# Kernel tuning notes

Hardware: AMD Instinct MI355X
Metric: run time of the kernel (lower is better)

## Reference

```python
import jax, jax.numpy as jnp
import numpy as np
import math

B, T, C = 2, 2048, 2048
H, KV, HD = 16, 4, 128          # n_head, n_kv_head, head_dim
REP = H // KV
FFN = 5632                      # multiple_of-rounded 2/3 * 4 * n_embd
EPS = 1e-5


def setup_inputs() -> dict:
    key = jax.random.key(0)
    ks = jax.random.split(key, 10)
    s = 0.02
    x = jax.random.normal(ks[0], (B, T, C), dtype=jnp.float32)
    # RoPE table: (T, HD/2, 2) = (cos, sin)
    inv_freq = 1.0 / (10000.0 ** (np.arange(0, HD, 2, dtype=np.float32) / HD))
    ang = np.arange(T, dtype=np.float32)[:, None] * inv_freq[None, :]
    freqs_cis = jnp.asarray(np.stack([np.cos(ang), np.sin(ang)], axis=-1))
    wq = s * jax.random.normal(ks[1], (H * HD, C), dtype=jnp.float32)
    wk = s * jax.random.normal(ks[2], (KV * HD, C), dtype=jnp.float32)
    wv = s * jax.random.normal(ks[3], (KV * HD, C), dtype=jnp.float32)
    wo = s * jax.random.normal(ks[4], (C, H * HD), dtype=jnp.float32)
    w1 = s * jax.random.normal(ks[5], (FFN, C), dtype=jnp.float32)
    w2 = s * jax.random.normal(ks[6], (FFN, C), dtype=jnp.float32)
    c_proj = s * jax.random.normal(ks[7], (C, FFN), dtype=jnp.float32)
    g1 = jnp.ones((C,), dtype=jnp.float32)
    g2 = jnp.ones((C,), dtype=jnp.float32)
    return {"x": x, "freqs_cis": freqs_cis, "wq": wq, "wk": wk, "wv": wv,
            "wo": wo, "w1": w1, "w2": w2, "c_proj": c_proj, "g1": g1, "g2": g2}


def _rmsnorm(x, g, eps=EPS):
    return x * jax.lax.rsqrt(jnp.mean(x * x, axis=-1, keepdims=True) + eps) * g


def _rope(t, freqs_cis):
    # t: (B, T, nH, HD); freqs_cis: (T, HD/2, 2)
    tr = t.reshape(*t.shape[:-1], HD // 2, 2)
    cos = freqs_cis[None, :, None, :, 0]
    sin = freqs_cis[None, :, None, :, 1]
    out = jnp.stack([tr[..., 0] * cos - tr[..., 1] * sin,
                     tr[..., 0] * sin + tr[..., 1] * cos], axis=-1)
    return out.reshape(t.shape)


def reference(x, freqs_cis, wq, wk, wv, wo, w1, w2, c_proj, g1, g2):
    h = _rmsnorm(x, g1)
    q = (h @ wq.T).reshape(B, T, H, HD)
    k = (h @ wk.T).reshape(B, T, KV, HD)
    v = (h @ wv.T).reshape(B, T, KV, HD)
    q = _rope(q, freqs_cis)
    k = _rope(k, freqs_cis)
    # GQA: group query heads by kv head; never materialize expanded K/V
    q = q.transpose(0, 2, 1, 3).reshape(B, KV, REP, T, HD)  # b g r q d
    k = k.transpose(0, 2, 1, 3)                              # b g k d
    v = v.transpose(0, 2, 1, 3)                              # b g k d
    scale = 1.0 / math.sqrt(HD)
    scores = jnp.einsum('bgrqd,bgkd->bgrqk', q, k) * scale
    causal = jnp.tril(jnp.ones((T, T), dtype=bool))
    scores = jnp.where(causal, scores, jnp.float32(-1e30))
    attn = jax.nn.softmax(scores, axis=-1)
    y = jnp.einsum('bgrqk,bgkd->bgrqd', attn, v)
    y = y.reshape(B, H, T, HD).transpose(0, 2, 1, 3).reshape(B, T, C)
    x = x + y @ wo.T
    h2 = _rmsnorm(x, g2)
    mlp = (jax.nn.silu(h2 @ w1.T) * (h2 @ w2.T)) @ c_proj.T
    return x + mlp
```

## Files before the change

kernel.cpp:

```cpp
#include <hip/hip_runtime.h>
#include <hip/hip_bf16.h>
#include <math.h>

#define TT   2048
#define CC   2048
#define NB   2
#define NH   16
#define NKV  4
#define HDIM 128
#define NFFN 5632

typedef __attribute__((ext_vector_type(8))) short     bf8;
typedef __attribute__((ext_vector_type(4))) float     f32x4;
typedef __attribute__((ext_vector_type(8))) unsigned short u16x8;
typedef __attribute__((ext_vector_type(4))) unsigned short u16x4;

__device__ __forceinline__ float b2f(unsigned short u) {
    union { unsigned u; float f; } v; v.u = ((unsigned)u) << 16; return v.f;
}
__device__ __forceinline__ unsigned short f2bf(float f) {
    union { float f; unsigned u; } v; v.f = f;
    unsigned r = (v.u + 0x7fffu + ((v.u >> 16) & 1u)) >> 16;
    return (unsigned short)r;
}
__device__ __forceinline__ void gll16(const void* g, void* l) {
    __builtin_amdgcn_global_load_lds((const __attribute__((address_space(1))) void*)g,
                                     (__attribute__((address_space(3))) void*)l, 16, 0, 0);
}

__global__ __launch_bounds__(256) void cvt_k(const float* __restrict__ in,
        __hip_bfloat16* __restrict__ out)
{
    const size_t i = ((size_t)blockIdx.x * 256 + threadIdx.x) * 8;
    float4 a = *(const float4*)(in + i);
    float4 b = *(const float4*)(in + i + 4);
    u16x8 v;
    v[0] = f2bf(a.x); v[1] = f2bf(a.y); v[2] = f2bf(a.z); v[3] = f2bf(a.w);
    v[4] = f2bf(b.x); v[5] = f2bf(b.y); v[6] = f2bf(b.z); v[7] = f2bf(b.w);
    *(u16x8*)((unsigned short*)out + i) = v;
}

__global__ __launch_bounds__(256) void cvt3_k(const float* __restrict__ wq,
        const float* __restrict__ wk, const float* __restrict__ wv,
        __hip_bfloat16* __restrict__ out)
{
    const int row = blockIdx.x;
    const float* src = (row < 2048) ? (wq + (size_t)row * CC)
                     : (row < 2560) ? (wk + (size_t)(row - 2048) * CC)
                                    : (wv + (size_t)(row - 2560) * CC);
    const int e0 = threadIdx.x * 8;
    float4 a = *(const float4*)(src + e0);
    float4 b = *(const float4*)(src + e0 + 4);
    u16x8 v;
    v[0] = f2bf(a.x); v[1] = f2bf(a.y); v[2] = f2bf(a.z); v[3] = f2bf(a.w);
    v[4] = f2bf(b.x); v[5] = f2bf(b.y); v[6] = f2bf(b.z); v[7] = f2bf(b.w);
    *(u16x8*)((unsigned short*)out + (size_t)row * CC + e0) = v;
}

__global__ __launch_bounds__(256) void cvt2_k(const float* __restrict__ w1,
        const float* __restrict__ w2,
        __hip_bfloat16* __restrict__ o1, __hip_bfloat16* __restrict__ o2)
{
    const int row = blockIdx.x;
    const float* src;
    unsigned short* dst;
    if (row < NFFN) { src = w1 + (size_t)row * CC; dst = (unsigned short*)o1 + (size_t)row * CC; }
    else            { src = w2 + (size_t)(row - NFFN) * CC; dst = (unsigned short*)o2 + (size_t)(row - NFFN) * CC; }
    const int e0 = threadIdx.x * 8;
    float4 a = *(const float4*)(src + e0);
    float4 b = *(const float4*)(src + e0 + 4);
    u16x8 v;
    v[0] = f2bf(a.x); v[1] = f2bf(a.y); v[2] = f2bf(a.z); v[3] = f2bf(a.w);
    v[4] = f2bf(b.x); v[5] = f2bf(b.y); v[6] = f2bf(b.z); v[7] = f2bf(b.w);
    *(u16x8*)(dst + e0) = v;
}

__global__ __launch_bounds__(256) void rms_f32_k(const float* __restrict__ x,
        const float* __restrict__ g, __hip_bfloat16* __restrict__ o)
{
    const size_t row = blockIdx.x;
    const int e0 = threadIdx.x * 8;
    float4 a = *(const float4*)(x + row * CC + e0);
    float4 b = *(const float4*)(x + row * CC + e0 + 4);
    float vals[8] = {a.x, a.y, a.z, a.w, b.x, b.y, b.z, b.w};
    float s = 0.f;
    #pragma unroll
    for (int e = 0; e < 8; ++e) s += vals[e] * vals[e];
    #pragma unroll
    for (int off = 32; off; off >>= 1) s += __shfl_xor(s, off);
    __shared__ float wsum[4];
    if ((threadIdx.x & 63) == 0) wsum[threadIdx.x >> 6] = s;
    __syncthreads();
    float scale = rsqrtf((wsum[0] + wsum[1] + wsum[2] + wsum[3]) * (1.0f / CC) + 1e-5f);
    float4 g0 = *(const float4*)(g + e0);
    float4 g1 = *(const float4*)(g + e0 + 4);
    float gs[8] = {g0.x, g0.y, g0.z, g0.w, g1.x, g1.y, g1.z, g1.w};
    u16x8 ov;
    #pragma unroll
    for (int e = 0; e < 8; ++e) ov[e] = f2bf(vals[e] * scale * gs[e]);
    *(u16x8*)((unsigned short*)o + row * CC + e0) = ov;
}

__global__ __launch_bounds__(256) void rms_bf16_k(const __hip_bfloat16* __restrict__ x,
        const float* __restrict__ g, __hip_bfloat16* __restrict__ o)
{
    const size_t row = blockIdx.x;
    const int e0 = threadIdx.x * 8;
    u16x8 xv = *(const u16x8*)((const unsigned short*)x + row * CC + e0);
    float vals[8];
    #pragma unroll
    for (int e = 0; e < 8; ++e) vals[e] = b2f(xv[e]);
    float s = 0.f;
    #pragma unroll
    for (int e = 0; e < 8; ++e) s += vals[e] * vals[e];
    #pragma unroll
    for (int off = 32; off; off >>= 1) s += __shfl_xor(s, off);
    __shared__ float wsum[4];
    if ((threadIdx.x & 63) == 0) wsum[threadIdx.x >> 6] = s;
    __syncthreads();
    float scale = rsqrtf((wsum[0] + wsum[1] + wsum[2] + wsum[3]) * (1.0f / CC) + 1e-5f);
    float4 g0 = *(const float4*)(g + e0);
    float4 g1 = *(const float4*)(g + e0 + 4);
    float gs[8] = {g0.x, g0.y, g0.z, g0.w, g1.x, g1.y, g1.z, g1.w};
    u16x8 ov;
    #pragma unroll
    for (int e = 0; e < 8; ++e) ov[e] = f2bf(vals[e] * scale * gs[e]);
    *(u16x8*)((unsigned short*)o + row * CC + e0) = ov;
}

#define GBM 128
#define GBN 128
#define GBK 32

template<int EPI, int OUTB>
__global__ __launch_bounds__(256) void gemm_db(
        const __hip_bfloat16* __restrict__ A,
        const __hip_bfloat16* __restrict__ W,
        const void* __restrict__ Rp,
        void* __restrict__ Cp,
        int M, int N, int K)
{
    __shared__ alignas(16) __hip_bfloat16 As[2][GBM][GBK];
    __shared__ alignas(16) __hip_bfloat16 Ws[2][GBN][GBK];
    const int tid  = threadIdx.x;
    const int lane = tid & 63;
    const int wid  = tid >> 6;
    const int wr = wid >> 1, wc = wid & 1;
    const int nwg = gridDim.x * gridDim.y;
    const int lin = blockIdx.y * gridDim.x + blockIdx.x;
    const int nlin = (lin & 7) * (nwg >> 3) + (lin >> 3);
    const int bxs = nlin % gridDim.x, bys = nlin / gridDim.x;
    const int bm = bys * GBM, bn = bxs * GBN;
    const int l4  = lane >> 2;
    const int lk8 = (lane & 3) * 8;
    const int fr  = lane & 15;
    const int fk  = (lane >> 4) * 8;

    f32x4 acc[4][4];
    #pragma unroll
    for (int m = 0; m < 4; ++m)
        #pragma unroll
        for (int n = 0; n < 4; ++n) acc[m][n] = (f32x4){0.f, 0.f, 0.f, 0.f};

    const __hip_bfloat16* ga0 = A + (size_t)(bm + wid * 32 + l4) * K + lk8;
    const __hip_bfloat16* ga1 = A + (size_t)(bm + wid * 32 + 16 + l4) * K + lk8;
    const __hip_bfloat16* gw0 = W + (size_t)(bn + wid * 32 + l4) * K + lk8;
    const __hip_bfloat16* gw1 = W + (size_t)(bn + wid * 32 + 16 + l4) * K + lk8;

    const int nt = K >> 5;
    gll16(ga0, &As[0][wid * 32][0]);
    gll16(ga1, &As[0][wid * 32 + 16][0]);
    gll16(gw0, &Ws[0][wid * 32][0]);
    gll16(gw1, &Ws[0][wid * 32 + 16][0]);

    #pragma unroll 2
    for (int t = 0; t < nt; ++t) {
        const int cur = t & 1;
        __syncthreads();
        if (t + 1 < nt) {
            const int k1 = (t + 1) << 5;
            const int nx = cur ^ 1;
            gll16(ga0 + k1, &As[nx][wid * 32][0]);
            gll16(ga1 + k1, &As[nx][wid * 32 + 16][0]);
            gll16(gw0 + k1, &Ws[nx][wid * 32][0]);
            gll16(gw1 + k1, &Ws[nx][wid * 32 + 16][0]);
        }
        bf8 af[4];
        #pragma unroll
        for (int m = 0; m < 4; ++m)
            af[m] = *(const bf8*)&As[cur][wr * 64 + m * 16 + fr][fk];
        #pragma unroll
        for (int n = 0; n < 4; ++n) {
            bf8 wf = *(const bf8*)&Ws[cur][wc * 64 + n * 16 + fr][fk];
            #pragma unroll
            for (int m = 0; m < 4; ++m)
                acc[m][n] = __builtin_amdgcn_mfma_f32_16x16x32_bf16(af[m], wf, acc[m][n], 0, 0, 0);
        }
    }

    const int rj = (lane >> 4) * 4;
    #pragma unroll
    for (int m = 0; m < 4; ++m) {
        #pragma unroll
        for (int j = 0; j < 4; ++j) {
            const size_t row = (size_t)(bm + wr * 64 + m * 16 + rj + j);
            #pragma unroll
            for (int n = 0; n < 4; ++n) {
                const size_t col = (size_t)(bn + wc * 64 + n * 16 + fr);
                float v = acc[m][n][j];
                if (EPI == 1) v += ((const float*)Rp)[row * N + col];
                if (EPI == 2) v += b2f(((const unsigned short*)Rp)[row * N + col]);
                if (EPI == 3) {
                    float gv = b2f(((const unsigned short*)Rp)[row * N + col]);
                    v = (gv / (1.0f + __expf(-gv))) * v;
                }
                if (OUTB) ((unsigned short*)Cp)[row * N + col] = f2bf(v);
                else      ((float*)Cp)[row * N + col] = v;
            }
        }
    }
}

__global__ __launch_bounds__(256) void gemm_qkv_db(
        const __hip_bfloat16* __restrict__ A,
        const __hip_bfloat16* __restrict__ W,
        const float* __restrict__ fc,
        __hip_bfloat16* __restrict__ qo,
        __hip_bfloat16* __restrict__ ko,
        __hip_bfloat16* __restrict__ vto,
        int M, int K)
{
    __shared__ alignas(16) __hip_bfloat16 As[2][GBM][GBK];
    __shared__ alignas(16) __hip_bfloat16 Ws[2][GBN][GBK];
    const int tid  = threadIdx.x;
    const int lane = tid & 63;
    const int wid  = tid >> 6;
    const int wr = wid >> 1, wc = wid & 1;
    const int nwg = gridDim.x * gridDim.y;
    const int lin = blockIdx.y * gridDim.x + blockIdx.x;
    const int nlin = (lin & 7) * (nwg >> 3) + (lin >> 3);
    const int bxs = nlin % gridDim.x, bys = nlin / gridDim.x;
    const int bm = bys * GBM, bn = bxs * GBN;
    const int l4  = lane >> 2;
    const int lk8 = (lane & 3) * 8;
    const int fr  = lane & 15;
    const int fk  = (lane >> 4) * 8;

    f32x4 acc[4][4];
    #pragma unroll
    for (int m = 0; m < 4; ++m)
        #pragma unroll
        for (int n = 0; n < 4; ++n) acc[m][n] = (f32x4){0.f, 0.f, 0.f, 0.f};

    const __hip_bfloat16* ga0 = A + (size_t)(bm + wid * 32 + l4) * K + lk8;
    const __hip_bfloat16* ga1 = A + (size_t)(bm + wid * 32 + 16 + l4) * K + lk8;
    const __hip_bfloat16* gw0 = W + (size_t)(bn + wid * 32 + l4) * K + lk8;
    const __hip_bfloat16* gw1 = W + (size_t)(bn + wid * 32 + 16 + l4) * K + lk8;

    const int nt = K >> 5;
    gll16(ga0, &As[0][wid * 32][0]);
    gll16(ga1, &As[0][wid * 32 + 16][0]);
    gll16(gw0, &Ws[0][wid * 32][0]);
    gll16(gw1, &Ws[0][wid * 32 + 16][0]);

    #pragma unroll 2
    for (int t = 0; t < nt; ++t) {
        const int cur = t & 1;
        __syncthreads();
        if (t + 1 < nt) {
            const int k1 = (t + 1) << 5;
            const int nx = cur ^ 1;
            gll16(ga0 + k1, &As[nx][wid * 32][0]);
            gll16(ga1 + k1, &As[nx][wid * 32 + 16][0]);
            gll16(gw0 + k1, &Ws[nx][wid * 32][0]);
            gll16(gw1 + k1, &Ws[nx][wid * 32 + 16][0]);
        }
        bf8 af[4];
        #pragma unroll
        for (int m = 0; m < 4; ++m)
            af[m] = *(const bf8*)&As[cur][wr * 64 + m * 16 + fr][fk];
        #pragma unroll
        for (int n = 0; n < 4; ++n) {
            bf8 wf = *(const bf8*)&Ws[cur][wc * 64 + n * 16 + fr][fk];
            #pragma unroll
            for (int m = 0; m < 4; ++m)
                acc[m][n] = __builtin_amdgcn_mfma_f32_16x16x32_bf16(af[m], wf, acc[m][n], 0, 0, 0);
        }
    }

    const int rj = (lane >> 4) * 4;
    #pragma unroll
    for (int m = 0; m < 4; ++m) {
        #pragma unroll
        for (int n = 0; n < 4; ++n) {
            const int col = bn + wc * 64 + n * 16 + fr;
            const int row0 = bm + wr * 64 + m * 16 + rj;
            if (col < 2560) {
                const int i2 = ((col & 127) >> 1) * 2;
                const int role = col & 1;
                #pragma unroll
                for (int j = 0; j < 4; ++j) {
                    const int t0 = (row0 + j) & (TT - 1);
                    const float cv = fc[t0 * HDIM + i2];
                    const float sv = fc[t0 * HDIM + i2 + 1];
                    const float v = acc[m][n][j];
                    const float partner = __shfl_xor(v, 1);
                    const float o = role ? (partner * sv + v * cv) : (v * cv - partner * sv);
                    if (col < 2048)
                        ((unsigned short*)qo)[(size_t)(row0 + j) * CC + col] = f2bf(o);
                    else
                        ((unsigned short*)ko)[(size_t)(row0 + j) * (NKV * HDIM) + (col - 2048)] = f2bf(o);
                }
            } else {
                const int vc = col - 2560;
                const int g = vc >> 7, d = vc & 127;
                const int b = row0 >> 11, t0 = row0 & (TT - 1);
                unsigned short* vp = (unsigned short*)vto +
                    ((size_t)(b * NKV + g) * HDIM + d) * TT + t0;
                u16x4 ov;
                #pragma unroll
                for (int j = 0; j < 4; ++j) ov[j] = f2bf(acc[m][n][j]);
                *(u16x4*)vp = ov;
            }
        }
    }
}

#define PBM 128
#define PBN 256
#define PBK 64

template<int EPI, int OUTB>
__global__ __launch_bounds__(512) void gemm_8p(
        const __hip_bfloat16* __restrict__ A,
        const __hip_bfloat16* __restrict__ W,
        const void* __restrict__ Rp,
        void* __restrict__ Cp,
        int M, int N, int K)
{
    __shared__ alignas(16) __hip_bfloat16 As[2][PBM][PBK];
    __shared__ alignas(16) __hip_bfloat16 Ws[2][PBN][PBK];
    const int tid  = threadIdx.x;
    const int lane = tid & 63;
    const int wid  = tid >> 6;
    const int wr = wid >> 2, wc = wid & 3;
    const int nwg = gridDim.x * gridDim.y;
    const int lin = blockIdx.y * gridDim.x + blockIdx.x;
    const int nlin = (lin & 7) * (nwg >> 3) + (lin >> 3);
    const int bxs = nlin % gridDim.x, bys = nlin / gridDim.x;
    const int bm = bys * PBM, bn = bxs * PBN;
    const int fr = lane & 15;
    const int hi = lane >> 4;

    f32x4 acc[4][4];
    #pragma unroll
    for (int m = 0; m < 4; ++m)
        #pragma unroll
        for (int n = 0; n < 4; ++n) acc[m][n] = (f32x4){0.f, 0.f, 0.f, 0.f};

    const unsigned short* Ag = (const unsigned short*)A;
    const unsigned short* Wg = (const unsigned short*)W;

    auto STAGE = [&](int buf, int k0) {
        #pragma unroll
        for (int l = 0; l < 2; ++l) {
            const int s = l * 512 + tid;
            const int row = s >> 3;
            const int srcb = ((s & 7) * 16) ^ ((row & 7) << 4);
            gll16(Ag + (size_t)(bm + row) * K + k0 + (srcb >> 1),
                  (unsigned short*)&As[buf][0][0] + (l * 512 + wid * 64) * 8);
        }
        #pragma unroll
        for (int l = 0; l < 4; ++l) {
            const int s = l * 512 + tid;
            const int row = s >> 3;
            const int srcb = ((s & 7) * 16) ^ ((row & 7) << 4);
            gll16(Wg + (size_t)(bn + row) * K + k0 + (srcb >> 1),
                  (unsigned short*)&Ws[buf][0][0] + (l * 512 + wid * 64) * 8);
        }
    };

    const int nt = K >> 6;
    STAGE(0, 0);
    __syncthreads();

    for (int t = 0; t < nt; ++t) {
        const int cur = t & 1;
        const char* Ab = (const char*)&As[cur][0][0];
        const char* Bb = (const char*)&Ws[cur][0][0];

        bf8 bF[4][2];
        #pragma unroll
        for (int n = 0; n < 4; ++n) {
            const int row = wc * 64 + n * 16 + fr;
            #pragma unroll
            for (int kk = 0; kk < 2; ++kk) {
                const int off = (kk * 64 + hi * 16) ^ ((row & 7) << 4);
                bF[n][kk] = *(const bf8*)(Bb + row * 128 + off);
            }
        }
        bf8 a0, a1;
        {
            const int row = wr * 64 + fr;
            a0 = *(const bf8*)(Ab + row * 128 + ((hi * 16)      ^ ((row & 7) << 4)));
            a1 = *(const bf8*)(Ab + row * 128 + ((64 + hi * 16) ^ ((row & 7) << 4)));
        }
        if (t + 1 < nt) STAGE(cur ^ 1, (t + 1) * PBK);
        __builtin_amdgcn_s_barrier();
        __builtin_amdgcn_s_setprio(1);
        #pragma unroll
        for (int n = 0; n < 4; ++n) {
            acc[0][n] = __builtin_amdgcn_mfma_f32_16x16x32_bf16(a0, bF[n][0], acc[0][n], 0, 0, 0);
            acc[0][n] = __builtin_amdgcn_mfma_f32_16x16x32_bf16(a1, bF[n][1], acc[0][n], 0, 0, 0);
        }
        __builtin_amdgcn_s_setprio(0);
        __builtin_amdgcn_s_barrier();

        #pragma unroll
        for (int m = 1; m < 4; ++m) {
            const int row = wr * 64 + m * 16 + fr;
            bf8 am0 = *(const bf8*)(Ab + row * 128 + ((hi * 16)      ^ ((row & 7) << 4)));
            bf8 am1 = *(const bf8*)(Ab + row * 128 + ((64 + hi * 16) ^ ((row & 7) << 4)));
            __builtin_amdgcn_s_barrier();
            __builtin_amdgcn_s_setprio(1);
            #pragma unroll
            for (int n = 0; n < 4; ++n) {
                acc[m][n] = __builtin_amdgcn_mfma_f32_16x16x32_bf16(am0, bF[n][0], acc[m][n], 0, 0, 0);
                acc[m][n] = __builtin_amdgcn_mfma_f32_16x16x32_bf16(am1, bF[n][1], acc[m][n], 0, 0, 0);
            }
            __builtin_amdgcn_s_setprio(0);
            if (m < 3) __builtin_amdgcn_s_barrier();
        }
        __syncthreads();
    }

    const int rj = hi * 4;
    #pragma unroll
    for (int m = 0; m < 4; ++m) {
        #pragma unroll
        for (int j = 0; j < 4; ++j) {
            const size_t row = (size_t)(bm + wr * 64 + m * 16 + rj + j);
            #pragma unroll
            for (int n = 0; n < 4; ++n) {
                const size_t col = (size_t)(bn + wc * 64 + n * 16 + fr);
                float v = acc[m][n][j];
                if (EPI == 1) v += ((const float*)Rp)[row * N + col];
                if (EPI == 2) v += b2f(((const unsigned short*)Rp)[row * N + col]);
                if (EPI == 3) {
                    float gv = b2f(((const unsigned short*)Rp)[row * N + col]);
                    v = (gv / (1.0f + __expf(-gv))) * v;
                }
                if (OUTB) ((unsigned short*)Cp)[row * N + col] = f2bf(v);
                else      ((float*)Cp)[row * N + col] = v;
            }
        }
    }
}

#define AQB 128
#define AKV 64

__global__ __launch_bounds__(512) void attn_mfma(const __hip_bfloat16* __restrict__ q,
        const __hip_bfloat16* __restrict__ k, const __hip_bfloat16* __restrict__ vt,
        __hip_bfloat16* __restrict__ y)
{
    __shared__ alignas(16) unsigned short Ks[AKV * HDIM];
    __shared__ alignas(16) unsigned short Vs[HDIM * AKV];
    __shared__ alignas(16) unsigned short Ps[AQB * AKV];

    const int qt = (TT / AQB - 1) - blockIdx.x;
    const int h  = blockIdx.y;
    const int b  = blockIdx.z;
    const int g  = h >> 2;
    const int qbase = qt * AQB;

    const int tid  = threadIdx.x;
    const int lane = tid & 63;
    const int wid  = tid >> 6;
    const int fr   = lane & 15;
    const int fk8  = (lane >> 4) * 8;
    const int rj   = (lane >> 4) * 4;

    bf8 qf[4];
    {
        const unsigned short* qp = (const unsigned short*)q +
            (size_t)(b * TT + qbase + wid * 16 + fr) * CC + h * HDIM;
        #pragma unroll
        for (int c = 0; c < 4; ++c)
            qf[c] = *(const bf8*)(qp + c * 32 + fk8);
    }
    const unsigned short* vtb = (const unsigned short*)vt + (size_t)(b * NKV + g) * HDIM * TT;

    f32x4 oacc[8];
    float m_r = -1e30f, l_r = 0.f;
    #pragma unroll
    for (int n = 0; n < 8; ++n) oacc[n] = (f32x4){0.f, 0.f, 0.f, 0.f};

    const float scale = 0.08838834764831845f;
    const int ntiles = qbase / AKV + 2;
    const int kjr = tid >> 3;
    const int kkc = (tid & 7) * 16;
    const int vdr = tid >> 2;
    const int vjc = (tid & 3) * 16;
    const int qg = qbase + wid * 16 + fr;
    const int prow = wid * 16 + fr;

    u16x8 krg[2], vrg[2];
    auto LOADT = [&](int jb) {
        const unsigned short* kp = (const unsigned short*)k +
            ((size_t)(b * TT + jb + kjr) * (NKV * HDIM)) + g * HDIM + kkc;
        const unsigned short* vp = vtb + (size_t)vdr * TT + jb + vjc;
        #pragma unroll
        for (int c = 0; c < 2; ++c) {
            krg[c] = *(const u16x8*)(kp + c * 8);
            vrg[c] = *(const u16x8*)(vp + c * 8);
        }
    };
    auto WRITET = [&]() {
        #pragma unroll
        for (int c = 0; c < 2; ++c) {
            const int byteK = (kjr * 256 + (kkc + c * 8) * 2) ^ ((kjr & 7) << 4);
            *(u16x8*)((char*)Ks + byteK) = krg[c];
            const int byteV = (vdr * 128 + (vjc + c * 8) * 2) ^ ((vdr & 7) << 4);
            *(u16x8*)((char*)Vs + byteV) = vrg[c];
        }
    };

    LOADT(0);

    for (int tile = 0; tile < ntiles; ++tile) {
        __syncthreads();
        WRITET();
        if (tile + 1 < ntiles) LOADT((tile + 1) * AKV);
        __syncthreads();

        f32x4 s[4];
        #pragma unroll
        for (int n = 0; n < 4; ++n) s[n] = (f32x4){0.f, 0.f, 0.f, 0.f};
        __builtin_amdgcn_s_setprio(1);
        #pragma unroll
        for (int c = 0; c < 4; ++c) {
            #pragma unroll
            for (int n = 0; n < 4; ++n) {
                const int j = n * 16 + fr;
                const int byteB = (j * 256 + (c * 32 + fk8) * 2) ^ ((j & 7) << 4);
                bf8 kf = *(const bf8*)((char*)Ks + byteB);
                s[n] = __builtin_amdgcn_mfma_f32_16x16x32_bf16(kf, qf[c], s[n], 0, 0, 0);
            }
        }
        __builtin_amdgcn_s_setprio(0);

        const int jbase = tile * AKV;
        float sv[4][4];
        float tmax = -1e30f;
        #pragma unroll
        for (int n = 0; n < 4; ++n)
            #pragma unroll
            for (int j = 0; j < 4; ++j) {
                const int jg = jbase + n * 16 + rj + j;
                sv[n][j] = (jg <= qg) ? s[n][j] * scale : -1e30f;
                tmax = fmaxf(tmax, sv[n][j]);
            }
        tmax = fmaxf(tmax, __shfl_xor(tmax, 16));
        tmax = fmaxf(tmax, __shfl_xor(tmax, 32));
        const bool trig = tmax > m_r + 8.0f;
        if (__any(trig)) {
            const float alpha = trig ? __expf(m_r - tmax) : 1.0f;
            if (trig) m_r = tmax;
            l_r *= alpha;
            float aj[4];
            #pragma unroll
            for (int j = 0; j < 4; ++j) aj[j] = __shfl(alpha, rj + j);
            #pragma unroll
            for (int n = 0; n < 8; ++n)
                #pragma unroll
                for (int j = 0; j < 4; ++j) oacc[n][j] *= aj[j];
        }
        float tsum = 0.f;
        #pragma unroll
        for (int n = 0; n < 4; ++n)
            #pragma unroll
            for (int j = 0; j < 4; ++j) {
                const float p = __expf(sv[n][j] - m_r);
                tsum += p;
                const int byteP = (prow * 128 + (n * 16 + rj + j) * 2) ^ ((prow & 7) << 4);
                *(unsigned short*)((char*)Ps + byteP) = f2bf(p);
            }
        tsum += __shfl_xor(tsum, 16);
        tsum += __shfl_xor(tsum, 32);
        l_r += tsum;

        __builtin_amdgcn_s_setprio(1);
        #pragma unroll
        for (int c2 = 0; c2 < 2; ++c2) {
            const int byteA = (prow * 128 + (c2 * 32 + fk8) * 2) ^ ((prow & 7) << 4);
            bf8 pf = *(const bf8*)((char*)Ps + byteA);
            #pragma unroll
            for (int n = 0; n < 8; ++n) {
                const int d = n * 16 + fr;
                const int byteB = (d * 128 + (c2 * 32 + fk8) * 2) ^ ((d & 7) << 4);
                bf8 vf = *(const bf8*)((char*)Vs + byteB);
                oacc[n] = __builtin_amdgcn_mfma_f32_16x16x32_bf16(pf, vf, oacc[n], 0, 0, 0);
            }
        }
        __builtin_amdgcn_s_setprio(0);
    }

    const float rl = 1.0f / l_r;
    #pragma unroll
    for (int jj = 0; jj < 4; ++jj) {
        const float inv = __shfl(rl, rj + jj);
        unsigned short* yrow = (unsigned short*)y +
            ((size_t)(b * TT + qbase + wid * 16 + rj + jj) * CC) + h * HDIM;
        #pragma unroll
        for (int n = 0; n < 8; ++n)
            yrow[n * 16 + fr] = f2bf(oacc[n][jj] * inv);
    }
}

extern "C" void kernel_launch(void* const* d_in, const int* in_sizes, int n_in,
                              void* d_out, int out_size, void* d_ws, size_t ws_size,
                              hipStream_t stream)
{
    (void)in_sizes; (void)n_in; (void)out_size; (void)ws_size;
    const float* x     = (const float*)d_in[0];
    const float* fc    = (const float*)d_in[1];
    const float* wq    = (const float*)d_in[2];
    const float* wk    = (const float*)d_in[3];
    const float* wv    = (const float*)d_in[4];
    const float* wo    = (const float*)d_in[5];
    const float* w1    = (const float*)d_in[6];
    const float* w2    = (const float*)d_in[7];
    const float* cproj = (const float*)d_in[8];
    const float* g1    = (const float*)d_in[9];
    const float* g2    = (const float*)d_in[10];
    float* out = (float*)d_out;

    const int ROWS = NB * TT;
    unsigned char* wsb = (unsigned char*)d_ws;
    __hip_bfloat16* x2b = (__hip_bfloat16*)(wsb);
    __hip_bfloat16* hb  = (__hip_bfloat16*)(wsb + 16777216u);
    __hip_bfloat16* w1b = (__hip_bfloat16*)(wsb + 33554432u);
    __hip_bfloat16* w2b = (__hip_bfloat16*)(wsb + 56623104u);
    __hip_bfloat16* G1  = (__hip_bfloat16*)(wsb + 79691776u);
    __hip_bfloat16* cpb = w1b;
    __hip_bfloat16* qb   = (__hip_bfloat16*)(wsb + 33554432u);
    __hip_bfloat16* kb   = (__hip_bfloat16*)(wsb + 50331648u);
    __hip_bfloat16* vtb  = (__hip_bfloat16*)(wsb + 54525952u);
    __hip_bfloat16* yb   = (__hip_bfloat16*)(wsb + 58720256u);
    __hip_bfloat16* wbuf = (__hip_bfloat16*)(wsb + 75497472u);

    rms_f32_k<<<ROWS, 256, 0, stream>>>(x, g1, hb);
    cvt3_k<<<3072, 256, 0, stream>>>(wq, wk, wv, wbuf);
    gemm_qkv_db<<<dim3(3072 / GBN, ROWS / GBM), 256, 0, stream>>>(hb, wbuf, fc, qb, kb, vtb, ROWS, CC);
    attn_mfma<<<dim3(TT / AQB, NH, NB), 512, 0, stream>>>(qb, kb, vtb, yb);
    cvt_k<<<(CC * CC) / 2048, 256, 0, stream>>>(wo, wbuf);
    gemm_8p<1, 1><<<dim3(CC / PBN, ROWS / PBM), 512, 0, stream>>>(yb, wbuf, x, x2b, ROWS, CC, CC);
    rms_bf16_k<<<ROWS, 256, 0, stream>>>(x2b, g2, hb);
    cvt2_k<<<2 * NFFN, 256, 0, stream>>>(w1, w2, w1b, w2b);
    gemm_8p<0, 1><<<dim3(NFFN / PBN, ROWS / PBM), 512, 0, stream>>>(hb, w1b, nullptr, G1, ROWS, NFFN, CC);
    gemm_8p<3, 1><<<dim3(NFFN / PBN, ROWS / PBM), 512, 0, stream>>>(hb, w2b, G1, G1, ROWS, NFFN, CC);
    cvt_k<<<(CC * NFFN) / 2048, 256, 0, stream>>>(cproj, cpb);
    gemm_8p<2, 0><<<dim3(CC / PBN, ROWS / PBM), 512, 0, stream>>>(G1, cpb, x2b, out, ROWS, CC, NFFN);
}
```

Before: 620.2 us.

## Port QKV GEMM to 8-wave pipelined kernel and double-buffer attention K/V tiles

The QKV projection GEMM moves from the 256-thread 128x128x32 double-buffered kernel to the 512-thread 128x256x64 design already used for the other GEMMs. That design uses swizzled LDS staging and interleaves barriers with MFMA groups. The old gemm_db is removed. The attention kernel now double-buffers its K/V shared-memory tiles and writes the next tile after the PV MFMAs, which drops one __syncthreads per tile and overlaps the LDS write with compute. In exchange, attention uses more LDS, and the QKV grid has fewer, larger blocks (12x32).

```diff
diff --git a/kernel.cpp b/kernel.cpp
--- a/kernel.cpp
+++ b/kernel.cpp
@@ -128,33 +128,31 @@
     *(u16x8*)((unsigned short*)o + row * CC + e0) = ov;
 }
 
-#define GBM 128
-#define GBN 128
-#define GBK 32
+#define PBM 128
+#define PBN 256
+#define PBK 64
 
 template<int EPI, int OUTB>
-__global__ __launch_bounds__(256) void gemm_db(
+__global__ __launch_bounds__(512) void gemm_8p(
         const __hip_bfloat16* __restrict__ A,
         const __hip_bfloat16* __restrict__ W,
         const void* __restrict__ Rp,
         void* __restrict__ Cp,
         int M, int N, int K)
 {
-    __shared__ alignas(16) __hip_bfloat16 As[2][GBM][GBK];
-    __shared__ alignas(16) __hip_bfloat16 Ws[2][GBN][GBK];
+    __shared__ alignas(16) __hip_bfloat16 As[2][PBM][PBK];
+    __shared__ alignas(16) __hip_bfloat16 Ws[2][PBN][PBK];
     const int tid  = threadIdx.x;
     const int lane = tid & 63;
     const int wid  = tid >> 6;
-    const int wr = wid >> 1, wc = wid & 1;
+    const int wr = wid >> 2, wc = wid & 3;
     const int nwg = gridDim.x * gridDim.y;
     const int lin = blockIdx.y * gridDim.x + blockIdx.x;
     const int nlin = (lin & 7) * (nwg >> 3) + (lin >> 3);
     const int bxs = nlin % gridDim.x, bys = nlin / gridDim.x;
-    const int bm = bys * GBM, bn = bxs * GBN;
-    const int l4  = lane >> 2;
-    const int lk8 = (lane & 3) * 8;
-    const int fr  = lane & 15;
-    const int fk  = (lane >> 4) * 8;
+    const int bm = bys * PBM, bn = bxs * PBN;
+    const int fr = lane & 15;
+    const int hi = lane >> 4;
 
     f32x4 acc[4][4];
     #pragma unroll
@@ -162,43 +160,83 @@
         #pragma unroll
         for (int n = 0; n < 4; ++n) acc[m][n] = (f32x4){0.f, 0.f, 0.f, 0.f};
 
-    const __hip_bfloat16* ga0 = A + (size_t)(bm + wid * 32 + l4) * K + lk8;
-    const __hip_bfloat16* ga1 = A + (size_t)(bm + wid * 32 + 16 + l4) * K + lk8;
-    const __hip_bfloat16* gw0 = W + (size_t)(bn + wid * 32 + l4) * K + lk8;
-    const __hip_bfloat16* gw1 = W + (size_t)(bn + wid * 32 + 16 + l4) * K + lk8;
-
-    const int nt = K >> 5;
-    gll16(ga0, &As[0][wid * 32][0]);
-    gll16(ga1, &As[0][wid * 32 + 16][0]);
-    gll16(gw0, &Ws[0][wid * 32][0]);
-    gll16(gw1, &Ws[0][wid * 32 + 16][0]);
-
-    #pragma unroll 2
+    const unsigned short* Ag = (const unsigned short*)A;
+    const unsigned short* Wg = (const unsigned short*)W;
+
+    auto STAGE = [&](int buf, int k0) {
+        #pragma unroll
+        for (int l = 0; l < 2; ++l) {
+            const int s = l * 512 + tid;
+            const int row = s >> 3;
+            const int srcb = ((s & 7) * 16) ^ ((row & 7) << 4);
+            gll16(Ag + (size_t)(bm + row) * K + k0 + (srcb >> 1),
+                  (unsigned short*)&As[buf][0][0] + (l * 512 + wid * 64) * 8);
+        }
+        #pragma unroll
+        for (int l = 0; l < 4; ++l) {
+            const int s = l * 512 + tid;
+            const int row = s >> 3;
+            const int srcb = ((s & 7) * 16) ^ ((row & 7) << 4);
+            gll16(Wg + (size_t)(bn + row) * K + k0 + (srcb >> 1),
+                  (unsigned short*)&Ws[buf][0][0] + (l * 512 + wid * 64) * 8);
+        }
+    };
+
+    const int nt = K >> 6;
+    STAGE(0, 0);
+    __syncthreads();
+
     for (int t = 0; t < nt; ++t) {
         const int cur = t & 1;
+        const char* Ab = (const char*)&As[cur][0][0];
+        const char* Bb = (const char*)&Ws[cur][0][0];
+
+        bf8 bF[4][2];
+        #pragma unroll
+        for (int n = 0; n < 4; ++n) {
+            const int row = wc * 64 + n * 16 + fr;
+            #pragma unroll
+            for (int kk = 0; kk < 2; ++kk) {
+                const int off = (kk * 64 + hi * 16) ^ ((row & 7) << 4);
+                bF[n][kk] = *(const bf8*)(Bb + row * 128 + off);
+            }
+        }
+        bf8 a0, a1;
+        {
+            const int row = wr * 64 + fr;
+            a0 = *(const bf8*)(Ab + row * 128 + ((hi * 16)      ^ ((row & 7) << 4)));
+            a1 = *(const bf8*)(Ab + row * 128 + ((64 + hi * 16) ^ ((row & 7) << 4)));
+        }
+        if (t + 1 < nt) STAGE(cur ^ 1, (t + 1) * PBK);
+        __builtin_amdgcn_s_barrier();
+        __builtin_amdgcn_s_setprio(1);
+        #pragma unroll
+        for (int n = 0; n < 4; ++n) {
+            acc[0][n] = __builtin_amdgcn_mfma_f32_16x16x32_bf16(a0, bF[n][0], acc[0][n], 0, 0, 0);
+            acc[0][n] = __builtin_amdgcn_mfma_f32_16x16x32_bf16(a1, bF[n][1], acc[0][n], 0, 0, 0);
+        }
+        __builtin_amdgcn_s_setprio(0);
+        __builtin_amdgcn_s_barrier();
+
+        #pragma unroll
+        for (int m = 1; m < 4; ++m) {
+            const int row = wr * 64 + m * 16 + fr;
+            bf8 am0 = *(const bf8*)(Ab + row * 128 + ((hi * 16)      ^ ((row & 7) << 4)));
+            bf8 am1 = *(const bf8*)(Ab + row * 128 + ((64 + hi * 16) ^ ((row & 7) << 4)));
+            __builtin_amdgcn_s_barrier();
+            __builtin_amdgcn_s_setprio(1);
+            #pragma unroll
+            for (int n = 0; n < 4; ++n) {
+                acc[m][n] = __builtin_amdgcn_mfma_f32_16x16x32_bf16(am0, bF[n][0], acc[m][n], 0, 0, 0);
+                acc[m][n] = __builtin_amdgcn_mfma_f32_16x16x32_bf16(am1, bF[n][1], acc[m][n], 0, 0, 0);
+            }
+            __builtin_amdgcn_s_setprio(0);
+            if (m < 3) __builtin_amdgcn_s_barrier();
+        }
         __syncthreads();
-        if (t + 1 < nt) {
-            const int k1 = (t + 1) << 5;
-            const int nx = cur ^ 1;
-            gll16(ga0 + k1, &As[nx][wid * 32][0]);
-            gll16(ga1 + k1, &As[nx][wid * 32 + 16][0]);
-            gll16(gw0 + k1, &Ws[nx][wid * 32][0]);
-            gll16(gw1 + k1, &Ws[nx][wid * 32 + 16][0]);
-        }
-        bf8 af[4];
-        #pragma unroll
-        for (int m = 0; m < 4; ++m)
-            af[m] = *(const bf8*)&As[cur][wr * 64 + m * 16 + fr][fk];
-        #pragma unroll
-        for (int n = 0; n < 4; ++n) {
-            bf8 wf = *(const bf8*)&Ws[cur][wc * 64 + n * 16 + fr][fk];
-            #pragma unroll
-            for (int m = 0; m < 4; ++m)
-                acc[m][n] = __builtin_amdgcn_mfma_f32_16x16x32_bf16(af[m], wf, acc[m][n], 0, 0, 0);
-        }
     }
 
-    const int rj = (lane >> 4) * 4;
+    const int rj = hi * 4;
     #pragma unroll
     for (int m = 0; m < 4; ++m) {
         #pragma unroll
@@ -221,7 +259,7 @@
     }
 }
 
-__global__ __launch_bounds__(256) void gemm_qkv_db(
+__global__ __launch_bounds__(512) void gemm_qkv_8p(
         const __hip_bfloat16* __restrict__ A,
         const __hip_bfloat16* __restrict__ W,
         const float* __restrict__ fc,
@@ -230,21 +268,19 @@
         __hip_bfloat16* __restrict__ vto,
         int M, int K)
 {
-    __shared__ alignas(16) __hip_bfloat16 As[2][GBM][GBK];
-    __shared__ alignas(16) __hip_bfloat16 Ws[2][GBN][GBK];
+    __shared__ alignas(16) __hip_bfloat16 As[2][PBM][PBK];
+    __shared__ alignas(16) __hip_bfloat16 Ws[2][PBN][PBK];
     const int tid  = threadIdx.x;
     const int lane = tid & 63;
     const int wid  = tid >> 6;
-    const int wr = wid >> 1, wc = wid & 1;
+    const int wr = wid >> 2, wc = wid & 3;
     const int nwg = gridDim.x * gridDim.y;
     const int lin = blockIdx.y * gridDim.x + blockIdx.x;
     const int nlin = (lin & 7) * (nwg >> 3) + (lin >> 3);
     const int bxs = nlin % gridDim.x, bys = nlin / gridDim.x;
-    const int bm = bys * GBM, bn = bxs * GBN;
-    const int l4  = lane >> 2;
-    const int lk8 = (lane & 3) * 8;
-    const int fr  = lane & 15;
-    const int fk  = (lane >> 4) * 8;
+    const int bm = bys * PBM, bn = bxs * PBN;
+    const int fr = lane & 15;
+    const int hi = lane >> 4;
 
     f32x4 acc[4][4];
     #pragma unroll
@@ -252,43 +288,83 @@
         #pragma unroll
         for (int n = 0; n < 4; ++n) acc[m][n] = (f32x4){0.f, 0.f, 0.f, 0.f};
 
-    const __hip_bfloat16* ga0 = A + (size_t)(bm + wid * 32 + l4) * K + lk8;
-    const __hip_bfloat16* ga1 = A + (size_t)(bm + wid * 32 + 16 + l4) * K + lk8;
-    const __hip_bfloat16* gw0 = W + (size_t)(bn + wid * 32 + l4) * K + lk8;
-    const __hip_bfloat16* gw1 = W + (size_t)(bn + wid * 32 + 16 + l4) * K + lk8;
-
-    const int nt = K >> 5;
-    gll16(ga0, &As[0][wid * 32][0]);
-    gll16(ga1, &As[0][wid * 32 + 16][0]);
-    gll16(gw0, &Ws[0][wid * 32][0]);
-    gll16(gw1, &Ws[0][wid * 32 + 16][0]);
-
-    #pragma unroll 2
+    const unsigned short* Ag = (const unsigned short*)A;
+    const unsigned short* Wg = (const unsigned short*)W;
+
+    auto STAGE = [&](int buf, int k0) {
+        #pragma unroll
+        for (int l = 0; l < 2; ++l) {
+            const int s = l * 512 + tid;
+            const int row = s >> 3;
+            const int srcb = ((s & 7) * 16) ^ ((row & 7) << 4);
+            gll16(Ag + (size_t)(bm + row) * K + k0 + (srcb >> 1),
+                  (unsigned short*)&As[buf][0][0] + (l * 512 + wid * 64) * 8);
+        }
+        #pragma unroll
+        for (int l = 0; l < 4; ++l) {
+            const int s = l * 512 + tid;
+            const int row = s >> 3;
+            const int srcb = ((s & 7) * 16) ^ ((row & 7) << 4);
+            gll16(Wg + (size_t)(bn + row) * K + k0 + (srcb >> 1),
+                  (unsigned short*)&Ws[buf][0][0] + (l * 512 + wid * 64) * 8);
+        }
+    };
+
+    const int nt = K >> 6;
+    STAGE(0, 0);
+    __syncthreads();
+
     for (int t = 0; t < nt; ++t) {
         const int cur = t & 1;
+        const char* Ab = (const char*)&As[cur][0][0];
+        const char* Bb = (const char*)&Ws[cur][0][0];
+
+        bf8 bF[4][2];
+        #pragma unroll
+        for (int n = 0; n < 4; ++n) {
+            const int row = wc * 64 + n * 16 + fr;
+            #pragma unroll
+            for (int kk = 0; kk < 2; ++kk) {
+                const int off = (kk * 64 + hi * 16) ^ ((row & 7) << 4);
+                bF[n][kk] = *(const bf8*)(Bb + row * 128 + off);
+            }
+        }
+        bf8 a0, a1;
+        {
+            const int row = wr * 64 + fr;
+            a0 = *(const bf8*)(Ab + row * 128 + ((hi * 16)      ^ ((row & 7) << 4)));
+            a1 = *(const bf8*)(Ab + row * 128 + ((64 + hi * 16) ^ ((row & 7) << 4)));
+        }
+        if (t + 1 < nt) STAGE(cur ^ 1, (t + 1) * PBK);
+        __builtin_amdgcn_s_barrier();
+        __builtin_amdgcn_s_setprio(1);
+        #pragma unroll
+        for (int n = 0; n < 4; ++n) {
+            acc[0][n] = __builtin_amdgcn_mfma_f32_16x16x32_bf16(a0, bF[n][0], acc[0][n], 0, 0, 0);
+            acc[0][n] = __builtin_amdgcn_mfma_f32_16x16x32_bf16(a1, bF[n][1], acc[0][n], 0, 0, 0);
+        }
+        __builtin_amdgcn_s_setprio(0);
+        __builtin_amdgcn_s_barrier();
+
+        #pragma unroll
+        for (int m = 1; m < 4; ++m) {
+            const int row = wr * 64 + m * 16 + fr;
+            bf8 am0 = *(const bf8*)(Ab + row * 128 + ((hi * 16)      ^ ((row & 7) << 4)));
+            bf8 am1 = *(const bf8*)(Ab + row * 128 + ((64 + hi * 16) ^ ((row & 7) << 4)));
+            __builtin_amdgcn_s_barrier();
+            __builtin_amdgcn_s_setprio(1);
+            #pragma unroll
+            for (int n = 0; n < 4; ++n) {
+                acc[m][n] = __builtin_amdgcn_mfma_f32_16x16x32_bf16(am0, bF[n][0], acc[m][n], 0, 0, 0);
+                acc[m][n] = __builtin_amdgcn_mfma_f32_16x16x32_bf16(am1, bF[n][1], acc[m][n], 0, 0, 0);
+            }
+            __builtin_amdgcn_s_setprio(0);
+            if (m < 3) __builtin_amdgcn_s_barrier();
+        }
         __syncthreads();
-        if (t + 1 < nt) {
-            const int k1 = (t + 1) << 5;
-            const int nx = cur ^ 1;
-            gll16(ga0 + k1, &As[nx][wid * 32][0]);
-            gll16(ga1 + k1, &As[nx][wid * 32 + 16][0]);
-            gll16(gw0 + k1, &Ws[nx][wid * 32][0]);
-            gll16(gw1 + k1, &Ws[nx][wid * 32 + 16][0]);
-        }
-        bf8 af[4];
-        #pragma unroll
-        for (int m = 0; m < 4; ++m)
-            af[m] = *(const bf8*)&As[cur][wr * 64 + m * 16 + fr][fk];
-        #pragma unroll
-        for (int n = 0; n < 4; ++n) {
-            bf8 wf = *(const bf8*)&Ws[cur][wc * 64 + n * 16 + fr][fk];
-            #pragma unroll
-            for (int m = 0; m < 4; ++m)
-                acc[m][n] = __builtin_amdgcn_mfma_f32_16x16x32_bf16(af[m], wf, acc[m][n], 0, 0, 0);
-        }
     }
 
-    const int rj = (lane >> 4) * 4;
+    const int rj = hi * 4;
     #pragma unroll
     for (int m = 0; m < 4; ++m) {
         #pragma unroll
@@ -326,137 +402,6 @@
     }
 }
 
-#define PBM 128
-#define PBN 256
-#define PBK 64
-
-template<int EPI, int OUTB>
-__global__ __launch_bounds__(512) void gemm_8p(
-        const __hip_bfloat16* __restrict__ A,
-        const __hip_bfloat16* __restrict__ W,
-        const void* __restrict__ Rp,
-        void* __restrict__ Cp,
-        int M, int N, int K)
-{
-    __shared__ alignas(16) __hip_bfloat16 As[2][PBM][PBK];
-    __shared__ alignas(16) __hip_bfloat16 Ws[2][PBN][PBK];
-    const int tid  = threadIdx.x;
-    const int lane = tid & 63;
-    const int wid  = tid >> 6;
-    const int wr = wid >> 2, wc = wid & 3;
-    const int nwg = gridDim.x * gridDim.y;
-    const int lin = blockIdx.y * gridDim.x + blockIdx.x;
-    const int nlin = (lin & 7) * (nwg >> 3) + (lin >> 3);
-    const int bxs = nlin % gridDim.x, bys = nlin / gridDim.x;
-    const int bm = bys * PBM, bn = bxs * PBN;
-    const int fr = lane & 15;
-    const int hi = lane >> 4;
-
-    f32x4 acc[4][4];
-    #pragma unroll
-    for (int m = 0; m < 4; ++m)
-        #pragma unroll
-        for (int n = 0; n < 4; ++n) acc[m][n] = (f32x4){0.f, 0.f, 0.f, 0.f};
-
-    const unsigned short* Ag = (const unsigned short*)A;
-    const unsigned short* Wg = (const unsigned short*)W;
-
-    auto STAGE = [&](int buf, int k0) {
-        #pragma unroll
-        for (int l = 0; l < 2; ++l) {
-            const int s = l * 512 + tid;
-            const int row = s >> 3;
-            const int srcb = ((s & 7) * 16) ^ ((row & 7) << 4);
-            gll16(Ag + (size_t)(bm + row) * K + k0 + (srcb >> 1),
-                  (unsigned short*)&As[buf][0][0] + (l * 512 + wid * 64) * 8);
-        }
-        #pragma unroll
-        for (int l = 0; l < 4; ++l) {
-            const int s = l * 512 + tid;
-            const int row = s >> 3;
-            const int srcb = ((s & 7) * 16) ^ ((row & 7) << 4);
-            gll16(Wg + (size_t)(bn + row) * K + k0 + (srcb >> 1),
-                  (unsigned short*)&Ws[buf][0][0] + (l * 512 + wid * 64) * 8);
-        }
-    };
-
-    const int nt = K >> 6;
-    STAGE(0, 0);
-    __syncthreads();
-
-    for (int t = 0; t < nt; ++t) {
-        const int cur = t & 1;
-        const char* Ab = (const char*)&As[cur][0][0];
-        const char* Bb = (const char*)&Ws[cur][0][0];
-
-        bf8 bF[4][2];
-        #pragma unroll
-        for (int n = 0; n < 4; ++n) {
-            const int row = wc * 64 + n * 16 + fr;
-            #pragma unroll
-            for (int kk = 0; kk < 2; ++kk) {
-                const int off = (kk * 64 + hi * 16) ^ ((row & 7) << 4);
-                bF[n][kk] = *(const bf8*)(Bb + row * 128 + off);
-            }
-        }
-        bf8 a0, a1;
-        {
-            const int row = wr * 64 + fr;
-            a0 = *(const bf8*)(Ab + row * 128 + ((hi * 16)      ^ ((row & 7) << 4)));
-            a1 = *(const bf8*)(Ab + row * 128 + ((64 + hi * 16) ^ ((row & 7) << 4)));
-        }
-        if (t + 1 < nt) STAGE(cur ^ 1, (t + 1) * PBK);
-        __builtin_amdgcn_s_barrier();
-        __builtin_amdgcn_s_setprio(1);
-        #pragma unroll
-        for (int n = 0; n < 4; ++n) {
-            acc[0][n] = __builtin_amdgcn_mfma_f32_16x16x32_bf16(a0, bF[n][0], acc[0][n], 0, 0, 0);
-            acc[0][n] = __builtin_amdgcn_mfma_f32_16x16x32_bf16(a1, bF[n][1], acc[0][n], 0, 0, 0);
-        }
-        __builtin_amdgcn_s_setprio(0);
-        __builtin_amdgcn_s_barrier();
-
-        #pragma unroll
-        for (int m = 1; m < 4; ++m) {
-            const int row = wr * 64 + m * 16 + fr;
-            bf8 am0 = *(const bf8*)(Ab + row * 128 + ((hi * 16)      ^ ((row & 7) << 4)));
-            bf8 am1 = *(const bf8*)(Ab + row * 128 + ((64 + hi * 16) ^ ((row & 7) << 4)));
-            __builtin_amdgcn_s_barrier();
-            __builtin_amdgcn_s_setprio(1);
-            #pragma unroll
-            for (int n = 0; n < 4; ++n) {
-                acc[m][n] = __builtin_amdgcn_mfma_f32_16x16x32_bf16(am0, bF[n][0], acc[m][n], 0, 0, 0);
-                acc[m][n] = __builtin_amdgcn_mfma_f32_16x16x32_bf16(am1, bF[n][1], acc[m][n], 0, 0, 0);
-            }
-            __builtin_amdgcn_s_setprio(0);
-            if (m < 3) __builtin_amdgcn_s_barrier();
-        }
-        __syncthreads();
-    }
-
-    const int rj = hi * 4;
-    #pragma unroll
-    for (int m = 0; m < 4; ++m) {
-        #pragma unroll
-        for (int j = 0; j < 4; ++j) {
-            const size_t row = (size_t)(bm + wr * 64 + m * 16 + rj + j);
-            #pragma unroll
-            for (int n = 0; n < 4; ++n) {
-                const size_t col = (size_t)(bn + wc * 64 + n * 16 + fr);
-                float v = acc[m][n][j];
-                if (EPI == 1) v += ((const float*)Rp)[row * N + col];
-                if (EPI == 2) v += b2f(((const unsigned short*)Rp)[row * N + col]);
-                if (EPI == 3) {
-                    float gv = b2f(((const unsigned short*)Rp)[row * N + col]);
-                    v = (gv / (1.0f + __expf(-gv))) * v;
-                }
-                if (OUTB) ((unsigned short*)Cp)[row * N + col] = f2bf(v);
-                else      ((float*)Cp)[row * N + col] = v;
-            }
-        }
-    }
-}
-
 #define AQB 128
 #define AKV 64
 
@@ -464,8 +409,8 @@
         const __hip_bfloat16* __restrict__ k, const __hip_bfloat16* __restrict__ vt,
         __hip_bfloat16* __restrict__ y)
 {
-    __shared__ alignas(16) unsigned short Ks[AKV * HDIM];
-    __shared__ alignas(16) unsigned short Vs[HDIM * AKV];
+    __shared__ alignas(16) unsigned short Ks[2][AKV * HDIM];
+    __shared__ alignas(16) unsigned short Vs[2][HDIM * AKV];
     __shared__ alignas(16) unsigned short Ps[AQB * AKV];
 
     const int qt = (TT / AQB - 1) - blockIdx.x;
@@ -516,21 +461,21 @@
             vrg[c] = *(const u16x8*)(vp + c * 8);
         }
     };
-    auto WRITET = [&]() {
+    auto WRITET = [&](int buf) {
         #pragma unroll
         for (int c = 0; c < 2; ++c) {
             const int byteK = (kjr * 256 + (kkc + c * 8) * 2) ^ ((kjr & 7) << 4);
-            *(u16x8*)((char*)Ks + byteK) = krg[c];
+            *(u16x8*)((char*)&Ks[buf][0] + byteK) = krg[c];
             const int byteV = (vdr * 128 + (vjc + c * 8) * 2) ^ ((vdr & 7) << 4);
-            *(u16x8*)((char*)Vs + byteV) = vrg[c];
+            *(u16x8*)((char*)&Vs[buf][0] + byteV) = vrg[c];
         }
     };
 
     LOADT(0);
+    WRITET(0);
 
     for (int tile = 0; tile < ntiles; ++tile) {
-        __syncthreads();
-        WRITET();
+        const int cur = tile & 1;
         if (tile + 1 < ntiles) LOADT((tile + 1) * AKV);
         __syncthreads();
 
@@ -544,7 +489,7 @@
             for (int n = 0; n < 4; ++n) {
                 const int j = n * 16 + fr;
                 const int byteB = (j * 256 + (c * 32 + fk8) * 2) ^ ((j & 7) << 4);
-                bf8 kf = *(const bf8*)((char*)Ks + byteB);
+                bf8 kf = *(const bf8*)((char*)&Ks[cur][0] + byteB);
                 s[n] = __builtin_amdgcn_mfma_f32_16x16x32_bf16(kf, qf[c], s[n], 0, 0, 0);
             }
         }
@@ -599,11 +544,13 @@
             for (int n = 0; n < 8; ++n) {
                 const int d = n * 16 + fr;
                 const int byteB = (d * 128 + (c2 * 32 + fk8) * 2) ^ ((d & 7) << 4);
-                bf8 vf = *(const bf8*)((char*)Vs + byteB);
+                bf8 vf = *(const bf8*)((char*)&Vs[cur][0] + byteB);
                 oacc[n] = __builtin_amdgcn_mfma_f32_16x16x32_bf16(pf, vf, oacc[n], 0, 0, 0);
             }
         }
         __builtin_amdgcn_s_setprio(0);
+
+        if (tile + 1 < ntiles) WRITET(cur ^ 1);
     }
 
     const float rl = 1.0f / l_r;
@@ -652,7 +599,7 @@
 
     rms_f32_k<<<ROWS, 256, 0, stream>>>(x, g1, hb);
     cvt3_k<<<3072, 256, 0, stream>>>(wq, wk, wv, wbuf);
-    gemm_qkv_db<<<dim3(3072 / GBN, ROWS / GBM), 256, 0, stream>>>(hb, wbuf, fc, qb, kb, vtb, ROWS, CC);
+    gemm_qkv_8p<<<dim3(3072 / PBN, ROWS / PBM), 512, 0, stream>>>(hb, wbuf, fc, qb, kb, vtb, ROWS, CC);
     attn_mfma<<<dim3(TT / AQB, NH, NB), 512, 0, stream>>>(qb, kb, vtb, yb);
     cvt_k<<<(CC * CC) / 2048, 256, 0, stream>>>(wo, wbuf);
     gemm_8p<1, 1><<<dim3(CC / PBN, ROWS / PBM), 512, 0, stream>>>(yb, wbuf, x, x2b, ROWS, CC, CC);
```

After: 644.4 us. 1.04x slower.
